# Performance work log

Hardware: AMD Instinct MI355X
Metric: run time of the kernel (lower is better)

## Reference

```python
import jax, jax.numpy as jnp
import numpy as np

D_MODEL = 1024
NUM_HEADS = 16
HEAD_DIM = D_MODEL // NUM_HEADS


def setup_inputs() -> dict:
    key = jax.random.key(0)
    ks = jax.random.split(key, 9)
    B, S = 2, 2048
    scale = 1.0 / np.sqrt(D_MODEL)
    inp = {
        "X": jax.random.normal(ks[0], (B, S, D_MODEL), dtype=jnp.float32),
        "Wq_w": jax.random.normal(ks[1], (D_MODEL, D_MODEL), dtype=jnp.float32) * scale,
        "Wq_b": jnp.zeros((D_MODEL,), dtype=jnp.float32),
        "Wk_w": jax.random.normal(ks[2], (D_MODEL, D_MODEL), dtype=jnp.float32) * scale,
        "Wk_b": jnp.zeros((D_MODEL,), dtype=jnp.float32),
        "Wv_w": jax.random.normal(ks[3], (D_MODEL, D_MODEL), dtype=jnp.float32) * scale,
        "Wv_b": jnp.zeros((D_MODEL,), dtype=jnp.float32),
        "Wo_w": jax.random.normal(ks[4], (D_MODEL, D_MODEL), dtype=jnp.float32) * scale,
        "Wo_b": jnp.zeros((D_MODEL,), dtype=jnp.float32),
    }
    return inp


def reference(X, Wq_w, Wq_b, Wk_w, Wk_b, Wv_w, Wv_b, Wo_w, Wo_b):
    B, S, D = X.shape
    H, Hd = NUM_HEADS, HEAD_DIM

    def proj(W, b):  # torch Linear: x @ W.T + b -> [B,H,S,Hd]
        y = jnp.einsum('bsd,ed->bse', X, W) + b
        return y.reshape(B, S, H, Hd).transpose(0, 2, 1, 3)

    Q = proj(Wq_w, Wq_b)
    K = proj(Wk_w, Wk_b)
    V = proj(Wv_w, Wv_b)

    scores = jnp.einsum('bhqd,bhkd->bhqk', Q, K) / np.sqrt(Hd)
    causal = jnp.tril(jnp.ones((S, S), dtype=bool))  # True where allowed
    scores = jnp.where(causal, scores, -jnp.inf)
    attn = jax.nn.softmax(scores, axis=-1)  # [B,H,S,S]

    A = jnp.einsum('bhqk,bhkd->bhqd', attn, V)
    A = A.transpose(0, 2, 1, 3).reshape(B, S, D)
    out = jnp.einsum('bsd,ed->bse', A, Wo_w) + Wo_b
    return out, attn
```

## Files before the change

kernel.cpp:

```cpp
#include <hip/hip_runtime.h>
#include <hip/hip_bf16.h>
#include <stdint.h>

#define D_MODEL 1024
#define NH 16
#define HD 64
#define BATCH 2
#define SEQ 2048
#define TOK (BATCH*SEQ)

typedef __attribute__((ext_vector_type(8))) short short8;
typedef __attribute__((ext_vector_type(4))) float floatx4;

__device__ __forceinline__ unsigned short f2bf(float f) {
    union { float f; unsigned u; } v; v.f = f;
    unsigned r = v.u + 0x7fffu + ((v.u >> 16) & 1u);
    return (unsigned short)(r >> 16);
}

__global__ __launch_bounds__(256)
void convert_all(const float* __restrict__ X,
                 const float* __restrict__ Wq, const float* __restrict__ Wk,
                 const float* __restrict__ Wv, const float* __restrict__ Wo,
                 unsigned short* __restrict__ dst) {
    size_t i = ((size_t)blockIdx.x * 256 + threadIdx.x) * 4;
    const float* src; size_t off;
    if (i < 4194304u)      { src = X;  off = 0; }
    else if (i < 5242880u) { src = Wq; off = 4194304u; }
    else if (i < 6291456u) { src = Wk; off = 5242880u; }
    else if (i < 7340032u) { src = Wv; off = 6291456u; }
    else                   { src = Wo; off = 7340032u; }
    float4 v = *(const float4*)(src + (i - off));
    ushort4 o;
    o.x = f2bf(v.x); o.y = f2bf(v.y); o.z = f2bf(v.z); o.w = f2bf(v.w);
    *(ushort4*)(dst + i) = o;
}

__global__ __launch_bounds__(256)
void gemm_qkv(const unsigned short* __restrict__ Xb,
              const unsigned short* __restrict__ Wqb,
              const unsigned short* __restrict__ Wkb,
              const unsigned short* __restrict__ Wvb,
              const float* __restrict__ bq, const float* __restrict__ bk,
              const float* __restrict__ bv,
              unsigned short* __restrict__ Q,
              unsigned short* __restrict__ Kt,
              unsigned short* __restrict__ Vt) {
    const int m0 = blockIdx.x * 128;
    const int n0 = blockIdx.y * 128;
    const int mat = n0 >> 10;
    const int nl0 = n0 & 1023;
    const unsigned short* Wp = (mat == 0) ? Wqb : (mat == 1) ? Wkb : Wvb;
    const float* bp = (mat == 0) ? bq : (mat == 1) ? bk : bv;

    __shared__ __attribute__((aligned(16))) unsigned short Al[128 * 40];
    __shared__ __attribute__((aligned(16))) unsigned short Bl[128 * 40];

    const int tid = threadIdx.x;
    const int wave = tid >> 6, lane = tid & 63;
    const int wm = (wave >> 1) * 64, wn = (wave & 1) * 64;
    const int lr = lane & 15, lk = lane >> 4;

    floatx4 acc[4][4];
#pragma unroll
    for (int i = 0; i < 4; i++)
#pragma unroll
        for (int j = 0; j < 4; j++) acc[i][j] = (floatx4){0.f, 0.f, 0.f, 0.f};

    for (int k0 = 0; k0 < 1024; k0 += 32) {
        __syncthreads();
#pragma unroll
        for (int c = tid; c < 512; c += 256) {
            int row = c >> 2, col = (c & 3) << 3;
            *(int4*)(Al + row * 40 + col) =
                *(const int4*)(Xb + (size_t)(m0 + row) * 1024 + k0 + col);
        }
#pragma unroll
        for (int c = tid; c < 512; c += 256) {
            int row = c >> 2, col = (c & 3) << 3;
            *(int4*)(Bl + row * 40 + col) =
                *(const int4*)(Wp + (size_t)(nl0 + row) * 1024 + k0 + col);
        }
        __syncthreads();
        short8 af[4], bf[4];
#pragma unroll
        for (int i = 0; i < 4; i++)
            af[i] = *(const short8*)(Al + (wm + i * 16 + lr) * 40 + lk * 8);
#pragma unroll
        for (int j = 0; j < 4; j++)
            bf[j] = *(const short8*)(Bl + (wn + j * 16 + lr) * 40 + lk * 8);
#pragma unroll
        for (int i = 0; i < 4; i++)
#pragma unroll
            for (int j = 0; j < 4; j++)
                acc[i][j] = __builtin_amdgcn_mfma_f32_16x16x32_bf16(af[i], bf[j], acc[i][j], 0, 0, 0);
    }

#pragma unroll
    for (int i = 0; i < 4; i++) {
#pragma unroll
        for (int j = 0; j < 4; j++) {
            int ncol = nl0 + wn + j * 16 + lr;
            int h = ncol >> 6, d = ncol & 63;
            float bias = bp[ncol];
#pragma unroll
            for (int r = 0; r < 4; r++) {
                int m = m0 + wm + i * 16 + lk * 4 + r;
                int b = m >> 11, s = m & 2047;
                unsigned short v16 = f2bf(acc[i][j][r] + bias);
                if (mat == 2) {
                    Vt[((size_t)(b * NH + h) * HD + d) * SEQ + s] = v16;
                } else if (mat == 0) {
                    Q[((size_t)(b * NH + h) * SEQ + s) * HD + d] = v16;
                } else {
                    Kt[((size_t)(b * NH + h) * SEQ + s) * HD + d] = v16;
                }
            }
        }
    }
}

__global__ __launch_bounds__(256)
void attn_fused(const unsigned short* __restrict__ Q,
                const unsigned short* __restrict__ K,
                const unsigned short* __restrict__ Vt,
                float* __restrict__ attn,
                unsigned short* __restrict__ Ab) {
    const int qt = blockIdx.x;
    const int h = blockIdx.y, b = blockIdx.z;
    const size_t headQK = (size_t)(b * NH + h) * SEQ * HD;
    const size_t headV  = (size_t)(b * NH + h) * HD * SEQ;
    const unsigned short* Qh = Q + headQK;
    const unsigned short* Kh = K + headQK;
    const unsigned short* Vh = Vt + headV;
    float* attnRow = attn + (size_t)(b * NH + h) * SEQ * SEQ;

    __shared__ __attribute__((aligned(16))) unsigned short Ql[64 * 72];
    __shared__ __attribute__((aligned(16))) unsigned short Kl[64 * 72];
    __shared__ __attribute__((aligned(16))) unsigned short Vl[64 * 72];
    __shared__ __attribute__((aligned(16))) unsigned short Pl[64 * 72];

    const int tid = threadIdx.x;
    const int wave = tid >> 6, lane = tid & 63;
    const int lr = lane & 15, lk = lane >> 4;
    const int q0 = qt * 64;
    const int qrow_l = wave * 16 + lk * 4;

    for (int c = tid; c < 512; c += 256) {
        int row = c >> 3, col = (c & 7) << 3;
        *(int4*)(Ql + row * 72 + col) = *(const int4*)(Qh + (size_t)(q0 + row) * HD + col);
    }

    const float NEG = -3.0e38f;
    float m_r[4] = {NEG, NEG, NEG, NEG};
    float l_r[4] = {0.f, 0.f, 0.f, 0.f};
    floatx4 oacc[4];
#pragma unroll
    for (int n = 0; n < 4; n++) oacc[n] = (floatx4){0.f, 0.f, 0.f, 0.f};

    for (int kt = 0; kt <= qt; ++kt) {
        __syncthreads();
        for (int c = tid; c < 512; c += 256) {
            int row = c >> 3, col = (c & 7) << 3;
            *(int4*)(Kl + row * 72 + col) =
                *(const int4*)(Kh + (size_t)(kt * 64 + row) * HD + col);
        }
        __syncthreads();
        short8 a0 = *(const short8*)(Ql + (wave * 16 + lr) * 72 + lk * 8);
        short8 a1 = *(const short8*)(Ql + (wave * 16 + lr) * 72 + 32 + lk * 8);
        floatx4 sf[4];
#pragma unroll
        for (int n = 0; n < 4; ++n) {
            short8 b0 = *(const short8*)(Kl + (n * 16 + lr) * 72 + lk * 8);
            short8 b1 = *(const short8*)(Kl + (n * 16 + lr) * 72 + 32 + lk * 8);
            floatx4 z = (floatx4){0.f, 0.f, 0.f, 0.f};
            z = __builtin_amdgcn_mfma_f32_16x16x32_bf16(a0, b0, z, 0, 0, 0);
            z = __builtin_amdgcn_mfma_f32_16x16x32_bf16(a1, b1, z, 0, 0, 0);
            sf[n] = z;
        }
#pragma unroll
        for (int n = 0; n < 4; ++n)
#pragma unroll
            for (int r = 0; r < 4; ++r) {
                float s = sf[n][r] * 0.125f;
                int kg = kt * 64 + n * 16 + lr;
                int qg = q0 + qrow_l + r;
                if (kt == qt && kg > qg) s = NEG;
                sf[n][r] = s;
                attnRow[(size_t)qg * SEQ + kg] = s;
            }
#pragma unroll
        for (int r = 0; r < 4; ++r) {
            float v = fmaxf(fmaxf(sf[0][r], sf[1][r]), fmaxf(sf[2][r], sf[3][r]));
            v = fmaxf(v, __shfl_xor(v, 1));
            v = fmaxf(v, __shfl_xor(v, 2));
            v = fmaxf(v, __shfl_xor(v, 4));
            v = fmaxf(v, __shfl_xor(v, 8));
            float mnew = fmaxf(m_r[r], v);
            float alpha = __expf(m_r[r] - mnew);
            float rs = __expf(sf[0][r] - mnew) + __expf(sf[1][r] - mnew) +
                       __expf(sf[2][r] - mnew) + __expf(sf[3][r] - mnew);
            rs += __shfl_xor(rs, 1); rs += __shfl_xor(rs, 2);
            rs += __shfl_xor(rs, 4); rs += __shfl_xor(rs, 8);
            l_r[r] = l_r[r] * alpha + rs;
            m_r[r] = mnew;
        }
    }

    float rl[4];
#pragma unroll
    for (int r = 0; r < 4; ++r) rl[r] = 1.0f / l_r[r];

    for (int kt = 0; kt <= qt; ++kt) {
        __syncthreads();
        for (int c = tid; c < 512; c += 256) {
            int row = c >> 3, col = (c & 7) << 3;
            *(int4*)(Vl + row * 72 + col) =
                *(const int4*)(Vh + (size_t)row * SEQ + kt * 64 + col);
        }
#pragma unroll
        for (int n = 0; n < 4; ++n)
#pragma unroll
            for (int r = 0; r < 4; ++r) {
                int kg = kt * 64 + n * 16 + lr;
                int qg = q0 + qrow_l + r;
                size_t idx = (size_t)qg * SEQ + kg;
                float p = __expf(attnRow[idx] - m_r[r]) * rl[r];
                attnRow[idx] = p;
                Pl[(qrow_l + r) * 72 + n * 16 + lr] = f2bf(p);
            }
        __syncthreads();
        short8 p0 = *(const short8*)(Pl + (wave * 16 + lr) * 72 + lk * 8);
        short8 p1 = *(const short8*)(Pl + (wave * 16 + lr) * 72 + 32 + lk * 8);
#pragma unroll
        for (int n = 0; n < 4; ++n) {
            short8 v0 = *(const short8*)(Vl + (n * 16 + lr) * 72 + lk * 8);
            short8 v1 = *(const short8*)(Vl + (n * 16 + lr) * 72 + 32 + lk * 8);
            oacc[n] = __builtin_amdgcn_mfma_f32_16x16x32_bf16(p0, v0, oacc[n], 0, 0, 0);
            oacc[n] = __builtin_amdgcn_mfma_f32_16x16x32_bf16(p1, v1, oacc[n], 0, 0, 0);
        }
    }

#pragma unroll
    for (int n = 0; n < 4; ++n)
#pragma unroll
        for (int r = 0; r < 4; ++r) {
            int sq = q0 + qrow_l + r;
            int d = n * 16 + lr;
            Ab[(size_t)(b * SEQ + sq) * D_MODEL + h * HD + d] = f2bf(oacc[n][r]);
        }

    int c0 = (qt + 1) * 64;
    int zc = SEQ - c0;
    if (zc > 0) {
        float4 z4 = {0.f, 0.f, 0.f, 0.f};
        int per_row = zc >> 2;
        for (int row = 0; row < 64; ++row) {
            float4* dstp = (float4*)(attnRow + (size_t)(q0 + row) * SEQ + c0);
            for (int c = tid; c < per_row; c += 256) dstp[c] = z4;
        }
    }
}

__global__ __launch_bounds__(256)
void gemm_out(const unsigned short* __restrict__ Ab,
              const unsigned short* __restrict__ Wob,
              const float* __restrict__ bo,
              float* __restrict__ out) {
    const int m0 = blockIdx.x * 128;
    const int n0 = blockIdx.y * 128;

    __shared__ __attribute__((aligned(16))) unsigned short Al[128 * 40];
    __shared__ __attribute__((aligned(16))) unsigned short Bl[128 * 40];

    const int tid = threadIdx.x;
    const int wave = tid >> 6, lane = tid & 63;
    const int wm = (wave >> 1) * 64, wn = (wave & 1) * 64;
    const int lr = lane & 15, lk = lane >> 4;

    floatx4 acc[4][4];
#pragma unroll
    for (int i = 0; i < 4; i++)
#pragma unroll
        for (int j = 0; j < 4; j++) acc[i][j] = (floatx4){0.f, 0.f, 0.f, 0.f};

    for (int k0 = 0; k0 < 1024; k0 += 32) {
        __syncthreads();
#pragma unroll
        for (int c = tid; c < 512; c += 256) {
            int row = c >> 2, col = (c & 3) << 3;
            *(int4*)(Al + row * 40 + col) =
                *(const int4*)(Ab + (size_t)(m0 + row) * 1024 + k0 + col);
        }
#pragma unroll
        for (int c = tid; c < 512; c += 256) {
            int row = c >> 2, col = (c & 3) << 3;
            *(int4*)(Bl + row * 40 + col) =
                *(const int4*)(Wob + (size_t)(n0 + row) * 1024 + k0 + col);
        }
        __syncthreads();
        short8 af[4], bf[4];
#pragma unroll
        for (int i = 0; i < 4; i++)
            af[i] = *(const short8*)(Al + (wm + i * 16 + lr) * 40 + lk * 8);
#pragma unroll
        for (int j = 0; j < 4; j++)
            bf[j] = *(const short8*)(Bl + (wn + j * 16 + lr) * 40 + lk * 8);
#pragma unroll
        for (int i = 0; i < 4; i++)
#pragma unroll
            for (int j = 0; j < 4; j++)
                acc[i][j] = __builtin_amdgcn_mfma_f32_16x16x32_bf16(af[i], bf[j], acc[i][j], 0, 0, 0);
    }

#pragma unroll
    for (int i = 0; i < 4; i++)
#pragma unroll
        for (int j = 0; j < 4; j++) {
            int n = n0 + wn + j * 16 + lr;
            float bias = bo[n];
#pragma unroll
            for (int r = 0; r < 4; r++) {
                int m = m0 + wm + i * 16 + lk * 4 + r;
                out[(size_t)m * 1024 + n] = acc[i][j][r] + bias;
            }
        }
}

extern "C" void kernel_launch(void* const* d_in, const int* in_sizes, int n_in,
                              void* d_out, int out_size, void* d_ws, size_t ws_size,
                              hipStream_t stream) {
    (void)in_sizes; (void)n_in; (void)out_size; (void)ws_size;
    const float* X  = (const float*)d_in[0];
    const float* Wq = (const float*)d_in[1];
    const float* bq = (const float*)d_in[2];
    const float* Wk = (const float*)d_in[3];
    const float* bk = (const float*)d_in[4];
    const float* Wv = (const float*)d_in[5];
    const float* bv = (const float*)d_in[6];
    const float* Wo = (const float*)d_in[7];
    const float* bo = (const float*)d_in[8];

    float* out  = (float*)d_out;
    float* attn = out + (size_t)TOK * D_MODEL;

    unsigned short* wsb = (unsigned short*)d_ws;
    unsigned short* Xb  = wsb;
    unsigned short* Wqb = wsb + 4194304u;
    unsigned short* Wkb = wsb + 5242880u;
    unsigned short* Wvb = wsb + 6291456u;
    unsigned short* Wob = wsb + 7340032u;
    unsigned short* Qb  = wsb + 8388608u;
    unsigned short* Kb  = wsb + 12582912u;
    unsigned short* Vtb = wsb + 16777216u;
    unsigned short* Abf = wsb + 20971520u;

    convert_all<<<8192, 256, 0, stream>>>(X, Wq, Wk, Wv, Wo, wsb);
    gemm_qkv<<<dim3(32, 24), 256, 0, stream>>>(Xb, Wqb, Wkb, Wvb, bq, bk, bv, Qb, Kb, Vtb);
    attn_fused<<<dim3(32, NH, BATCH), 256, 0, stream>>>(Qb, Kb, Vtb, attn, Abf);
    gemm_out<<<dim3(32, 8), 256, 0, stream>>>(Abf, Wob, bo, out);
}
```

Measured before the change: 932.3 us.

## Recompute QK^T in second pass instead of round-tripping scores through attn output

```diff
diff --git a/kernel.cpp b/kernel.cpp
--- a/kernel.cpp
+++ b/kernel.cpp
@@ -44,14 +44,15 @@
               const float* __restrict__ bq, const float* __restrict__ bk,
               const float* __restrict__ bv,
               unsigned short* __restrict__ Q,
-              unsigned short* __restrict__ Kt,
-              unsigned short* __restrict__ Vt) {
+              unsigned short* __restrict__ Kb,
+              unsigned short* __restrict__ Vr) {
     const int m0 = blockIdx.x * 128;
     const int n0 = blockIdx.y * 128;
     const int mat = n0 >> 10;
     const int nl0 = n0 & 1023;
     const unsigned short* Wp = (mat == 0) ? Wqb : (mat == 1) ? Wkb : Wvb;
     const float* bp = (mat == 0) ? bq : (mat == 1) ? bk : bv;
+    unsigned short* Dst = (mat == 0) ? Q : (mat == 1) ? Kb : Vr;
 
     __shared__ __attribute__((aligned(16))) unsigned short Al[128 * 40];
     __shared__ __attribute__((aligned(16))) unsigned short Bl[128 * 40];
@@ -107,16 +108,38 @@
             for (int r = 0; r < 4; r++) {
                 int m = m0 + wm + i * 16 + lk * 4 + r;
                 int b = m >> 11, s = m & 2047;
-                unsigned short v16 = f2bf(acc[i][j][r] + bias);
-                if (mat == 2) {
-                    Vt[((size_t)(b * NH + h) * HD + d) * SEQ + s] = v16;
-                } else if (mat == 0) {
-                    Q[((size_t)(b * NH + h) * SEQ + s) * HD + d] = v16;
-                } else {
-                    Kt[((size_t)(b * NH + h) * SEQ + s) * HD + d] = v16;
-                }
+                Dst[((size_t)(b * NH + h) * SEQ + s) * HD + d] = f2bf(acc[i][j][r] + bias);
             }
         }
+    }
+}
+
+__global__ __launch_bounds__(256)
+void transpose_v(const unsigned short* __restrict__ Vr,
+                 unsigned short* __restrict__ Vt) {
+    const int st = blockIdx.x;
+    const int bh = blockIdx.y;
+    const int s0 = st * 64;
+    const unsigned short* src = Vr + (size_t)bh * SEQ * HD;
+    unsigned short* dst = Vt + (size_t)bh * HD * SEQ;
+
+    __shared__ __attribute__((aligned(16))) unsigned short Tl[64 * 72];
+    const int tid = threadIdx.x;
+
+#pragma unroll
+    for (int c = tid; c < 512; c += 256) {
+        int row = c >> 3, col = (c & 7) << 3;
+        *(int4*)(Tl + row * 72 + col) =
+            *(const int4*)(src + (size_t)(s0 + row) * HD + col);
+    }
+    __syncthreads();
+#pragma unroll
+    for (int c = tid; c < 512; c += 256) {
+        int d = c >> 3, sc = (c & 7) << 3;
+        short8 v;
+#pragma unroll
+        for (int j = 0; j < 8; ++j) v[j] = (short)Tl[(sc + j) * 72 + d];
+        *(short8*)(dst + (size_t)d * SEQ + s0 + sc) = v;
     }
 }
 
@@ -126,7 +149,7 @@
                 const unsigned short* __restrict__ Vt,
                 float* __restrict__ attn,
                 unsigned short* __restrict__ Ab) {
-    const int qt = blockIdx.x;
+    const int qt = 31 - blockIdx.x;
     const int h = blockIdx.y, b = blockIdx.z;
     const size_t headQK = (size_t)(b * NH + h) * SEQ * HD;
     const size_t headV  = (size_t)(b * NH + h) * HD * SEQ;
@@ -150,6 +173,9 @@
         int row = c >> 3, col = (c & 7) << 3;
         *(int4*)(Ql + row * 72 + col) = *(const int4*)(Qh + (size_t)(q0 + row) * HD + col);
     }
+    __syncthreads();
+    const short8 a0 = *(const short8*)(Ql + (wave * 16 + lr) * 72 + lk * 8);
+    const short8 a1 = *(const short8*)(Ql + (wave * 16 + lr) * 72 + 32 + lk * 8);
 
     const float NEG = -3.0e38f;
     float m_r[4] = {NEG, NEG, NEG, NEG};
@@ -166,8 +192,6 @@
                 *(const int4*)(Kh + (size_t)(kt * 64 + row) * HD + col);
         }
         __syncthreads();
-        short8 a0 = *(const short8*)(Ql + (wave * 16 + lr) * 72 + lk * 8);
-        short8 a1 = *(const short8*)(Ql + (wave * 16 + lr) * 72 + 32 + lk * 8);
         floatx4 sf[4];
 #pragma unroll
         for (int n = 0; n < 4; ++n) {
@@ -187,7 +211,6 @@
                 int qg = q0 + qrow_l + r;
                 if (kt == qt && kg > qg) s = NEG;
                 sf[n][r] = s;
-                attnRow[(size_t)qg * SEQ + kg] = s;
             }
 #pragma unroll
         for (int r = 0; r < 4; ++r) {
@@ -215,20 +238,30 @@
         __syncthreads();
         for (int c = tid; c < 512; c += 256) {
             int row = c >> 3, col = (c & 7) << 3;
+            *(int4*)(Kl + row * 72 + col) =
+                *(const int4*)(Kh + (size_t)(kt * 64 + row) * HD + col);
             *(int4*)(Vl + row * 72 + col) =
                 *(const int4*)(Vh + (size_t)row * SEQ + kt * 64 + col);
         }
-#pragma unroll
-        for (int n = 0; n < 4; ++n)
+        __syncthreads();
+#pragma unroll
+        for (int n = 0; n < 4; ++n) {
+            short8 b0 = *(const short8*)(Kl + (n * 16 + lr) * 72 + lk * 8);
+            short8 b1 = *(const short8*)(Kl + (n * 16 + lr) * 72 + 32 + lk * 8);
+            floatx4 z = (floatx4){0.f, 0.f, 0.f, 0.f};
+            z = __builtin_amdgcn_mfma_f32_16x16x32_bf16(a0, b0, z, 0, 0, 0);
+            z = __builtin_amdgcn_mfma_f32_16x16x32_bf16(a1, b1, z, 0, 0, 0);
 #pragma unroll
             for (int r = 0; r < 4; ++r) {
+                float s = z[r] * 0.125f;
                 int kg = kt * 64 + n * 16 + lr;
                 int qg = q0 + qrow_l + r;
-                size_t idx = (size_t)qg * SEQ + kg;
-                float p = __expf(attnRow[idx] - m_r[r]) * rl[r];
-                attnRow[idx] = p;
+                if (kt == qt && kg > qg) s = NEG;
+                float p = __expf(s - m_r[r]) * rl[r];
+                attnRow[(size_t)qg * SEQ + kg] = p;
                 Pl[(qrow_l + r) * 72 + n * 16 + lr] = f2bf(p);
             }
+        }
         __syncthreads();
         short8 p0 = *(const short8*)(Pl + (wave * 16 + lr) * 72 + lk * 8);
         short8 p1 = *(const short8*)(Pl + (wave * 16 + lr) * 72 + 32 + lk * 8);
@@ -352,11 +385,13 @@
     unsigned short* Wob = wsb + 7340032u;
     unsigned short* Qb  = wsb + 8388608u;
     unsigned short* Kb  = wsb + 12582912u;
-    unsigned short* Vtb = wsb + 16777216u;
+    unsigned short* Vrb = wsb + 16777216u;
     unsigned short* Abf = wsb + 20971520u;
+    unsigned short* Vtb = Xb;
 
     convert_all<<<8192, 256, 0, stream>>>(X, Wq, Wk, Wv, Wo, wsb);
-    gemm_qkv<<<dim3(32, 24), 256, 0, stream>>>(Xb, Wqb, Wkb, Wvb, bq, bk, bv, Qb, Kb, Vtb);
+    gemm_qkv<<<dim3(32, 24), 256, 0, stream>>>(Xb, Wqb, Wkb, Wvb, bq, bk, bv, Qb, Kb, Vrb);
+    transpose_v<<<dim3(32, 32), 256, 0, stream>>>(Vrb, Vtb);
     attn_fused<<<dim3(32, NH, BATCH), 256, 0, stream>>>(Qb, Kb, Vtb, attn, Abf);
     gemm_out<<<dim3(32, 8), 256, 0, stream>>>(Abf, Wob, bo, out);
 }
```

New measurement: 779.2 us. 16.4% less time.
